# Kernel tuning notes

Hardware: AMD Instinct MI355X
Metric: run time of the kernel (lower is better)

The kernel has to match this reference:

```python
import jax, jax.numpy as jnp
import numpy as np

EPS = 1e-5

def instance_norm(x):
    # x: [B, n, C]; InstanceNorm1d normalizes over the n (length) axis per channel, no affine
    mean = jnp.mean(x, axis=1, keepdims=True)
    var = jnp.var(x, axis=1, keepdims=True)  # biased variance, matches torch
    return (x - mean) / jnp.sqrt(var + EPS)

def gat_layer(h, w, a_src, a_dst, b):
    # h: [B, n, d_in]; w: [H, d_in, d_out]; a_src/a_dst: [H, d_out, 1]; b: [d_out]
    h_ = jnp.einsum('bnd,hdk->bhnk', h, w)               # [B, H, n, d_out]
    s_src = jnp.einsum('bhnk,hk->bhn', h_, a_src[..., 0])  # [B, H, n]
    s_dst = jnp.einsum('bhnk,hk->bhn', h_, a_dst[..., 0])  # [B, H, n]
    attn = s_src[:, :, :, None] + s_dst[:, :, None, :]    # [B, H, n, n]
    attn = jax.nn.leaky_relu(attn, negative_slope=0.2)
    attn = jax.nn.softmax(attn, axis=-1)
    return jnp.einsum('bhnm,bhmk->bhnk', attn, h_) + b    # [B, H, n, d_out]

def setup_inputs() -> dict:
    key = jax.random.key(0)
    ks = jax.random.split(key, 7)
    B, N = 4, 4096
    x = jax.random.normal(ks[0], (B, N, 64), dtype=jnp.float32)
    g = 1.414
    def xavier(k, shape):
        fan_in, fan_out = shape[-2], shape[-1]
        lim = g * np.sqrt(6.0 / (fan_in + fan_out))
        return jax.random.uniform(k, shape, jnp.float32, -lim, lim)
    return {
        'x': x,
        'w0': xavier(ks[1], (4, 64, 32)),
        'a_src0': xavier(ks[2], (4, 32, 1)),
        'a_dst0': xavier(ks[3], (4, 32, 1)),
        'b0': jnp.zeros((32,), jnp.float32),
        'w1': xavier(ks[4], (1, 128, 64)),
        'a_src1': xavier(ks[5], (1, 64, 1)),
        'a_dst1': xavier(ks[6], (1, 64, 1)),
        'b1': jnp.zeros((64,), jnp.float32),
    }

def reference(x, w0, a_src0, a_dst0, b0, w1, a_src1, a_dst1, b1):
    B, N = x.shape[:2]
    # layer 0: norm -> GAT(4 heads) -> concat heads -> ELU
    h = instance_norm(x)
    h = gat_layer(h, w0, a_src0, a_dst0, b0)              # [B, 4, N, 32]
    h = jnp.transpose(h, (0, 2, 1, 3)).reshape(B, N, -1)  # [B, N, 128]
    h = jax.nn.elu(h)
    # layer 1: norm -> GAT(1 head) -> squeeze head
    h = instance_norm(h)
    h = gat_layer(h, w1, a_src1, a_dst1, b1)              # [B, 1, N, 64]
    return h[:, 0]                                        # [B, N, 64]
```

## Files before the change

kernel.cpp:

```cpp
#include <hip/hip_runtime.h>
#include <math.h>

#define N_ 4096

static constexpr size_t OFF_STATS0 = 0;
static constexpr size_t OFF_STATS1 = 512;
static constexpr size_t OFF_HP0    = 2048;
static constexpr size_t OFF_ELU    = 2048;
static constexpr size_t OFF_SS0    = 2099200;
static constexpr size_t OFF_SD0    = 2164736;
static constexpr size_t OFF_RUNS0  = 2230272;
static constexpr size_t OFF_SV0    = 2361344;
static constexpr size_t OFF_PM0    = 2426880;
static constexpr size_t OFF_EP0    = 2492416;
static constexpr size_t OFF_EN0    = 2557952;
static constexpr size_t OFF_CPP0   = 2623488;
static constexpr size_t OFF_CPN0   = 2689040;
static constexpr size_t OFF_RAWP0  = 2754592;
static constexpr size_t OFF_RAWN0  = 2885664;
static constexpr size_t OFF_BP0    = 3016736;
static constexpr size_t OFF_BN0    = 3148320;
static constexpr size_t OFF_TPP0   = 3279904;
static constexpr size_t OFF_TPN0   = 5377568;
static constexpr size_t OFF_HP1    = 3279904;
static constexpr size_t OFF_SS1    = 4328480;
static constexpr size_t OFF_SD1    = 4344864;
static constexpr size_t OFF_RUNS1  = 4361248;
static constexpr size_t OFF_SV1    = 4394016;
static constexpr size_t OFF_PM1    = 4410400;
static constexpr size_t OFF_EP1    = 4426784;
static constexpr size_t OFF_EN1    = 4443168;
static constexpr size_t OFF_CPP1   = 4459552;
static constexpr size_t OFF_CPN1   = 4475940;
static constexpr size_t OFF_RAWP1  = 4492328;
static constexpr size_t OFF_RAWN1  = 4557864;
static constexpr size_t OFF_BP1    = 4623400;
static constexpr size_t OFF_BN1    = 4689192;
static constexpr size_t OFF_TPP1   = 4754984;
static constexpr size_t OFF_TPN1   = 5803816;

__device__ __forceinline__ unsigned f2s(float f){
  unsigned u=__float_as_uint(f);
  return u^((u&0x80000000u)?0xFFFFFFFFu:0x80000000u);
}
__device__ __forceinline__ float s2f(unsigned s){
  unsigned u=(s&0x80000000u)?(s^0x80000000u):~s;
  return __uint_as_float(u);
}

template<int C>
__global__ void kstats(const float* __restrict__ x, float* __restrict__ stats){
  int blk=blockIdx.x; int b=blk>>5, seg=blk&31;
  int tid=threadIdx.x;
  const int RPT=256/C;
  const int IT=128/RPT;
  int c=tid%C, rl=tid/C;
  const float* xb=x+(size_t)b*N_*C;
  float s1=0.f,s2=0.f;
  int r0=seg*128+rl;
  for(int i=0;i<IT;i++){
    float v=xb[(size_t)(r0+i*RPT)*C+c];
    s1+=v;s2+=v*v;
  }
  __shared__ float sh1[256],sh2[256];
  sh1[tid]=s1;sh2[tid]=s2;__syncthreads();
  if(tid<C){
    float a1=0.f,a2=0.f;
    for(int g=0;g<RPT;g++){a1+=sh1[g*C+tid];a2+=sh2[g*C+tid];}
    atomicAdd(&stats[(size_t)(b*C+tid)*2+0],a1);
    atomicAdd(&stats[(size_t)(b*C+tid)*2+1],a2);
  }
}

__global__ void __launch_bounds__(256) kproj0(
                       const float* __restrict__ x, const float* __restrict__ stats,
                       const float* __restrict__ w0, const float* __restrict__ asrc,
                       const float* __restrict__ adst, float* __restrict__ hp,
                       float* __restrict__ ss, float* __restrict__ sd){
  __shared__ float4 w4[2048];
  __shared__ float4 av4[64];
  __shared__ float mean[64],rstd[64];
  int tid=threadIdx.x;
  const float4* wg=(const float4*)w0;
  for(int i=tid;i<2048;i+=256) w4[i]=wg[i];
  if(tid<32) av4[tid]=((const float4*)asrc)[tid];
  else if(tid<64) av4[tid]=((const float4*)adst)[tid-32];
  int gid=blockIdx.x*256+tid;
  int b=gid>>14, h=(gid>>12)&3, n=gid&4095;
  if(tid<64){
    float s1=stats[(size_t)(b*64+tid)*2+0],s2=stats[(size_t)(b*64+tid)*2+1];
    float mu=s1*(1.0f/N_);
    float var=s2*(1.0f/N_)-mu*mu;
    mean[tid]=mu; rstd[tid]=rsqrtf(var+1e-5f);
  }
  __syncthreads();
  const float4* hr4=(const float4*)(x+((size_t)(b*N_+n))*64);
  float4 acc[8];
  #pragma unroll
  for(int q=0;q<8;q++) acc[q]=make_float4(0.f,0.f,0.f,0.f);
  #pragma unroll
  for(int ch=0;ch<4;ch++){
    float4 t[4];
    #pragma unroll
    for(int j=0;j<4;j++) t[j]=hr4[ch*4+j];
    #pragma unroll
    for(int j=0;j<4;j++){
      int d0=ch*16+j*4;
      float hv[4];
      hv[0]=(t[j].x-mean[d0+0])*rstd[d0+0];
      hv[1]=(t[j].y-mean[d0+1])*rstd[d0+1];
      hv[2]=(t[j].z-mean[d0+2])*rstd[d0+2];
      hv[3]=(t[j].w-mean[d0+3])*rstd[d0+3];
      #pragma unroll
      for(int dd=0;dd<4;dd++){
        float hvv=hv[dd];
        #pragma unroll
        for(int q=0;q<8;q++){
          float4 wv=w4[(h*64+d0+dd)*8+q];
          acc[q].x+=hvv*wv.x;acc[q].y+=hvv*wv.y;acc[q].z+=hvv*wv.z;acc[q].w+=hvv*wv.w;
        }
      }
    }
  }
  float ssv=0.f,sdv=0.f;
  #pragma unroll
  for(int q=0;q<8;q++){
    float4 a1=av4[h*8+q],a2=av4[32+h*8+q];
    ssv+=acc[q].x*a1.x+acc[q].y*a1.y+acc[q].z*a1.z+acc[q].w*a1.w;
    sdv+=acc[q].x*a2.x+acc[q].y*a2.y+acc[q].z*a2.z+acc[q].w*a2.w;
  }
  int p=b*4+h;
  float4* o4=(float4*)(hp+((size_t)p*N_+n)*32);
  #pragma unroll
  for(int q=0;q<8;q++) o4[q]=acc[q];
  ss[(size_t)p*N_+n]=ssv; sd[(size_t)p*N_+n]=sdv;
}

__global__ void __launch_bounds__(256) kproj1(
                       const float* __restrict__ x, const float* __restrict__ stats,
                       const float* __restrict__ w1, const float* __restrict__ asrc,
                       const float* __restrict__ adst, float* __restrict__ hp,
                       float* __restrict__ ss, float* __restrict__ sd){
  __shared__ float4 w4[2048];
  __shared__ float wa[128],wd[128],mean[128],rstd[128];
  int tid=threadIdx.x;
  const float4* wg=(const float4*)w1;
  for(int i=tid;i<2048;i+=256) w4[i]=wg[i];
  int gid=blockIdx.x*256+tid;
  int b=gid>>14, q4=(gid>>12)&3, n=gid&4095;
  if(tid<128){
    float s1a=0.f,s2a=0.f;
    for(int k=0;k<64;k++){float wv=w1[tid*64+k];s1a+=wv*asrc[k];s2a+=wv*adst[k];}
    wa[tid]=s1a;wd[tid]=s2a;
    float s1=stats[(size_t)(b*128+tid)*2+0],s2=stats[(size_t)(b*128+tid)*2+1];
    float mu=s1*(1.0f/N_);
    float var=s2*(1.0f/N_)-mu*mu;
    mean[tid]=mu; rstd[tid]=rsqrtf(var+1e-5f);
  }
  __syncthreads();
  const float4* hr4=(const float4*)(x+((size_t)(b*N_+n))*128);
  float4 acc[4];
  #pragma unroll
  for(int q=0;q<4;q++) acc[q]=make_float4(0.f,0.f,0.f,0.f);
  float s1=0.f,s2=0.f;
  #pragma unroll
  for(int ch=0;ch<8;ch++){
    float4 t[4];
    #pragma unroll
    for(int j=0;j<4;j++) t[j]=hr4[ch*4+j];
    #pragma unroll
    for(int j=0;j<4;j++){
      int d0=ch*16+j*4;
      float hv[4];
      hv[0]=(t[j].x-mean[d0+0])*rstd[d0+0];
      hv[1]=(t[j].y-mean[d0+1])*rstd[d0+1];
      hv[2]=(t[j].z-mean[d0+2])*rstd[d0+2];
      hv[3]=(t[j].w-mean[d0+3])*rstd[d0+3];
      #pragma unroll
      for(int dd=0;dd<4;dd++){
        float hvv=hv[dd]; int d=d0+dd;
        s1+=hvv*wa[d]; s2+=hvv*wd[d];
        #pragma unroll
        for(int q=0;q<4;q++){
          float4 wv=w4[d*16+q4*4+q];
          acc[q].x+=hvv*wv.x;acc[q].y+=hvv*wv.y;acc[q].z+=hvv*wv.z;acc[q].w+=hvv*wv.w;
        }
      }
    }
  }
  float4* o4=(float4*)(hp+((size_t)(b*N_+n))*64+q4*16);
  #pragma unroll
  for(int q=0;q<4;q++) o4[q]=acc[q];
  if(q4==0){
    ss[(size_t)b*N_+n]=s1;sd[(size_t)b*N_+n]=s2;
  }
}

__global__ void __launch_bounds__(256) ksort_runs(const float* __restrict__ sdst,
                                                  unsigned long long* __restrict__ runs){
  __shared__ unsigned long long sm[1024];
  int p=blockIdx.x>>2, run=blockIdx.x&3;
  int tid=threadIdx.x;
  const float* s=sdst+(size_t)p*N_+run*1024;
  for(int l=tid;l<1024;l+=256){
    unsigned key=f2s(s[l]);
    sm[l]=((unsigned long long)key<<32)|(unsigned)(run*1024+l);
  }
  for(unsigned k=2;k<=1024u;k<<=1)
    for(unsigned j=k>>1;j>0;j>>=1){
      __syncthreads();
      for(unsigned t=tid;t<512u;t+=256u){
        unsigned i=((t&~(j-1))<<1)|(t&(j-1));
        unsigned q=i|j;
        bool up=((i&k)==0);
        unsigned long long a=sm[i],b=sm[q];
        if((a>b)==up){sm[i]=b;sm[q]=a;}
      }
    }
  __syncthreads();
  unsigned long long* rg=runs+(size_t)p*N_+run*1024;
  for(int l=tid;l<1024;l+=256) rg[l]=sm[l];
}

__global__ void __launch_bounds__(1024) kmerge(const unsigned long long* __restrict__ runs,
    float* __restrict__ sv, unsigned* __restrict__ perm,
    float* __restrict__ eP, float* __restrict__ eN){
  __shared__ unsigned long long sm[4096];
  int p=blockIdx.x>>2, cg=blockIdx.x&3;
  int tid=threadIdx.x;
  const unsigned long long* rg=runs+(size_t)p*N_;
  for(int l=tid;l<4096;l+=1024) sm[l]=rg[l];
  __syncthreads();
  unsigned long long e=sm[cg*1024+tid];
  int rank=tid;
  #pragma unroll
  for(int o=0;o<4;o++){
    if(o==cg) continue;
    const unsigned long long* base=sm+o*1024;
    int lo=0,hi=1024;
    while(lo<hi){int mid=(lo+hi)>>1; if(base[mid]<e) lo=mid+1; else hi=mid;}
    rank+=lo;
  }
  unsigned long long mk=sm[1023];
  if(sm[2047]>mk) mk=sm[2047];
  if(sm[3071]>mk) mk=sm[3071];
  if(sm[4095]>mk) mk=sm[4095];
  float m=s2f((unsigned)(mk>>32));
  float v=s2f((unsigned)(e>>32));
  size_t o=(size_t)p*N_+rank;
  sv[o]=v;
  perm[o]=(unsigned)(e&0xffffffffu);
  eP[o]=expf(v-m);
  eN[o]=expf(0.2f*(v-m));
}

__global__ void __launch_bounds__(1024) kcounts(const float* __restrict__ eP,
    const float* __restrict__ eN, float* __restrict__ CPP, float* __restrict__ CPN){
  __shared__ float sp[1024],sn[1024];
  int p=blockIdx.x, t=threadIdx.x;
  float4 e4=((const float4*)(eP+(size_t)p*N_))[t];
  float4 n4=((const float4*)(eN+(size_t)p*N_))[t];
  float lp=e4.x+e4.y+e4.z+e4.w;
  float ln=n4.x+n4.y+n4.z+n4.w;
  sp[t]=lp; sn[t]=ln; __syncthreads();
  for(int off=1;off<1024;off<<=1){
    float vp=(t>=off)?sp[t-off]:0.f;
    float vn=(t>=off)?sn[t-off]:0.f;
    __syncthreads();
    sp[t]+=vp; sn[t]+=vn;
    __syncthreads();
  }
  float bp=sp[t]-lp, bn=sn[t]-ln;
  size_t o=(size_t)p*4097+t*4;
  float a=bp;          CPP[o+0]=a;
  a+=e4.x;             CPP[o+1]=a;
  a+=e4.y;             CPP[o+2]=a;
  a+=e4.z;             CPP[o+3]=a;
  a=bn;                CPN[o+0]=a;
  a+=n4.x;             CPN[o+1]=a;
  a+=n4.y;             CPN[o+2]=a;
  a+=n4.z;             CPN[o+3]=a;
  if(t==1023){CPP[(size_t)p*4097+4096]=sp[1023]; CPN[(size_t)p*4097+4096]=sn[1023];}
}

__global__ void __launch_bounds__(256) ktables0(const unsigned* __restrict__ perm,
    const float* __restrict__ eP, const float* __restrict__ eN,
    const float* __restrict__ hp, float* __restrict__ TPP, float* __restrict__ TPN,
    float* __restrict__ rawP, float* __restrict__ rawN){
  int gw=(blockIdx.x*256+threadIdx.x)>>6;
  int lane=threadIdx.x&63, half=lane>>5, ch=lane&31;
  int cglob=gw*2+half;
  int p=cglob>>8, c=cglob&255;
  float aP=0.f,aN=0.f;
  for(int q=0;q<16;q++){
    int r=c*16+q;
    size_t ro=(size_t)p*N_+r;
    float ep=eP[ro],en=eN[ro];
    unsigned pr=perm[ro];
    float hv=hp[((size_t)p*N_+pr)*32+ch];
    size_t to=((size_t)p*4097+r)*32+ch;
    TPP[to]=aP; TPN[to]=aN;
    aP+=ep*hv; aN+=en*hv;
  }
  size_t bo=((size_t)p*256+c)*32+ch;
  rawP[bo]=aP; rawN[bo]=aN;
}

__global__ void __launch_bounds__(256) ktables1(const unsigned* __restrict__ perm,
    const float* __restrict__ eP, const float* __restrict__ eN,
    const float* __restrict__ hp, float* __restrict__ TPP, float* __restrict__ TPN,
    float* __restrict__ rawP, float* __restrict__ rawN){
  int wid=(blockIdx.x*256+threadIdx.x)>>6;
  int lane=threadIdx.x&63;
  int p=wid>>8, c=wid&255;
  float aP=0.f,aN=0.f;
  for(int q=0;q<16;q++){
    int r=c*16+q;
    size_t ro=(size_t)p*N_+r;
    float ep=eP[ro],en=eN[ro];
    unsigned pr=perm[ro];
    float hv=hp[((size_t)p*N_+pr)*64+lane];
    size_t to=((size_t)p*4097+r)*64+lane;
    TPP[to]=aP; TPN[to]=aN;
    aP+=ep*hv; aN+=en*hv;
  }
  size_t bo=((size_t)p*256+c)*64+lane;
  rawP[bo]=aP; rawN[bo]=aN;
}

template<int D>
__global__ void __launch_bounds__(256) kscan(const float* __restrict__ rawP,
    const float* __restrict__ rawN, float* __restrict__ bP, float* __restrict__ bN,
    float* __restrict__ TPP, float* __restrict__ TPN){
  extern __shared__ float sm[];
  int p=blockIdx.x, tid=threadIdx.x;
  for(int pass=0;pass<2;pass++){
    const float* src=pass?rawN:rawP;
    float* dst=pass?bN:bP;
    float* tp=pass?TPN:TPP;
    __syncthreads();
    for(int i=tid;i<256*D;i+=256){
      sm[i]=src[(size_t)p*256*D+i];
    }
    __syncthreads();
    if(tid<D){
      float r=0.f;
      for(int c=0;c<256;c++){
        dst[((size_t)p*257+c)*D+tid]=r;
        r+=sm[c*D+tid];
      }
      dst[((size_t)p*257+256)*D+tid]=0.f;
      tp[((size_t)p*4097+4096)*D+tid]=r;
    }
  }
}

__global__ void __launch_bounds__(256) keval0(const float* __restrict__ ss,
                       const float* __restrict__ sv,
                       const float* __restrict__ bP, const float* __restrict__ bN,
                       const float* __restrict__ TPP, const float* __restrict__ TPN,
                       const float* __restrict__ CPP, const float* __restrict__ CPN,
                       const float* __restrict__ bias, float* __restrict__ out){
  int gw=(blockIdx.x*256+threadIdx.x)>>6;
  int lane=threadIdx.x&63, half=lane>>5, ch=lane&31;
  int row=gw*2+half;
  int p=row>>12, i=row&4095;
  int b=p>>2, h=p&3;
  const float* svp=sv+(size_t)p*N_;
  float ssrc=ss[(size_t)p*N_+i];
  float m=svp[4095];
  float xx=ssrc+m;
  float M=xx>0.f?xx:0.2f*xx;
  float fpos=expf(xx-M),fneg=expf(0.2f*xx-M);
  float th=-ssrc;
  float s1v=svp[ch*128+127];
  unsigned long long bal=__ballot(s1v<=th);
  int c1=half?(int)__popcll(bal>>32):(int)__popcll(bal&0xFFFFFFFFull);
  int lo;
  if(c1>=32){ lo=4096; }
  else{
    float s2v=svp[c1*128+ch*4+3];
    unsigned long long bal2=__ballot(s2v<=th);
    int c2=half?(int)__popcll(bal2>>32):(int)__popcll(bal2&0xFFFFFFFFull);
    int base=c1*128+c2*4;
    float4 qv=*((const float4*)(svp+base));
    int c3=(qv.x<=th)+(qv.y<=th)+(qv.z<=th)+(qv.w<=th);
    lo=base+c3;
  }
  int c=lo>>4;
  float relP=TPP[((size_t)p*4097+lo)*32+ch];
  float relN=TPN[((size_t)p*4097+lo)*32+ch];
  float baP=bP[((size_t)p*257+c)*32+ch];
  float baN=bN[((size_t)p*257+c)*32+ch];
  float tot=TPP[((size_t)p*4097+4096)*32+ch];
  float CPl=CPP[(size_t)p*4097+lo];
  float CNl=CPN[(size_t)p*4097+lo];
  float CT =CPP[(size_t)p*4097+4096];
  float denom=fpos*(CT-CPl)+fneg*CNl;
  float v=fpos*(tot-(baP+relP))+fneg*(baN+relN);
  float r=v/denom+bias[ch];
  r=r>0.f?r:expm1f(r);
  out[((size_t)(b*N_+i))*128+h*32+ch]=r;
}

__global__ void __launch_bounds__(256) keval1(const float* __restrict__ ss,
                       const float* __restrict__ sv,
                       const float* __restrict__ bP, const float* __restrict__ bN,
                       const float* __restrict__ TPP, const float* __restrict__ TPN,
                       const float* __restrict__ CPP, const float* __restrict__ CPN,
                       const float* __restrict__ bias, float* __restrict__ out){
  int wid=(blockIdx.x*256+threadIdx.x)>>6;
  int lane=threadIdx.x&63;
  int p=wid>>12, i=wid&4095;
  const float* svp=sv+(size_t)p*N_;
  float ssrc=ss[(size_t)p*N_+i];
  float m=svp[4095];
  float xx=ssrc+m;
  float M=xx>0.f?xx:0.2f*xx;
  float fpos=expf(xx-M),fneg=expf(0.2f*xx-M);
  float th=-ssrc;
  float s1v=svp[lane*64+63];
  int c1=(int)__popcll(__ballot(s1v<=th));
  int lo;
  if(c1>=64){ lo=4096; }
  else{
    float s2v=svp[c1*64+lane];
    lo=c1*64+(int)__popcll(__ballot(s2v<=th));
  }
  int c=lo>>4;
  float relP=TPP[((size_t)p*4097+lo)*64+lane];
  float relN=TPN[((size_t)p*4097+lo)*64+lane];
  float baP=bP[((size_t)p*257+c)*64+lane];
  float baN=bN[((size_t)p*257+c)*64+lane];
  float tot=TPP[((size_t)p*4097+4096)*64+lane];
  float CPl=CPP[(size_t)p*4097+lo];
  float CNl=CPN[(size_t)p*4097+lo];
  float CT =CPP[(size_t)p*4097+4096];
  float denom=fpos*(CT-CPl)+fneg*CNl;
  float v=fpos*(tot-(baP+relP))+fneg*(baN+relN);
  out[((size_t)p*N_+i)*64+lane]=v/denom+bias[lane];
}

extern "C" void kernel_launch(void* const* d_in, const int* in_sizes, int n_in,
                              void* d_out, int out_size, void* d_ws, size_t ws_size,
                              hipStream_t stream) {
  const float* x  =(const float*)d_in[0];
  const float* w0 =(const float*)d_in[1];
  const float* as0=(const float*)d_in[2];
  const float* ad0=(const float*)d_in[3];
  const float* b0 =(const float*)d_in[4];
  const float* w1 =(const float*)d_in[5];
  const float* as1=(const float*)d_in[6];
  const float* ad1=(const float*)d_in[7];
  const float* b1 =(const float*)d_in[8];
  float* ws=(float*)d_ws;
  float* out=(float*)d_out;

  float* st0 = ws+OFF_STATS0;
  float* st1 = ws+OFF_STATS1;
  float* hp0 = ws+OFF_HP0;
  float* elu = ws+OFF_ELU;
  float* ss0 = ws+OFF_SS0;  float* sd0 = ws+OFF_SD0;
  unsigned long long* runs0=(unsigned long long*)(ws+OFF_RUNS0);
  float* sv0 = ws+OFF_SV0;
  unsigned* pm0=(unsigned*)(ws+OFF_PM0);
  float* eP0 = ws+OFF_EP0;  float* eN0 = ws+OFF_EN0;
  float* cP0 = ws+OFF_CPP0; float* cN0 = ws+OFF_CPN0;
  float* rP0 = ws+OFF_RAWP0; float* rN0 = ws+OFF_RAWN0;
  float* bP0 = ws+OFF_BP0;  float* bN0 = ws+OFF_BN0;
  float* tP0 = ws+OFF_TPP0; float* tN0 = ws+OFF_TPN0;
  float* hp1 = ws+OFF_HP1;
  float* ss1 = ws+OFF_SS1;  float* sd1 = ws+OFF_SD1;
  unsigned long long* runs1=(unsigned long long*)(ws+OFF_RUNS1);
  float* sv1 = ws+OFF_SV1;
  unsigned* pm1=(unsigned*)(ws+OFF_PM1);
  float* eP1 = ws+OFF_EP1;  float* eN1 = ws+OFF_EN1;
  float* cP1 = ws+OFF_CPP1; float* cN1 = ws+OFF_CPN1;
  float* rP1 = ws+OFF_RAWP1; float* rN1 = ws+OFF_RAWN1;
  float* bP1 = ws+OFF_BP1;  float* bN1 = ws+OFF_BN1;
  float* tP1 = ws+OFF_TPP1; float* tN1 = ws+OFF_TPN1;

  hipMemsetAsync(d_ws, 0, 1536*sizeof(float), stream);

  kstats<64><<<128,256,0,stream>>>(x,st0);
  kproj0<<<256,256,0,stream>>>(x,st0,w0,as0,ad0,hp0,ss0,sd0);
  ksort_runs<<<64,256,0,stream>>>(sd0,runs0);
  kmerge<<<64,1024,0,stream>>>(runs0,sv0,pm0,eP0,eN0);
  kcounts<<<16,1024,0,stream>>>(eP0,eN0,cP0,cN0);
  ktables0<<<512,256,0,stream>>>(pm0,eP0,eN0,hp0,tP0,tN0,rP0,rN0);
  kscan<32><<<16,256,256*32*4,stream>>>(rP0,rN0,bP0,bN0,tP0,tN0);
  keval0<<<8192,256,0,stream>>>(ss0,sv0,bP0,bN0,tP0,tN0,cP0,cN0,b0,elu);
  kstats<128><<<128,256,0,stream>>>(elu,st1);
  kproj1<<<256,256,0,stream>>>(elu,st1,w1,as1,ad1,hp1,ss1,sd1);
  ksort_runs<<<16,256,0,stream>>>(sd1,runs1);
  kmerge<<<16,1024,0,stream>>>(runs1,sv1,pm1,eP1,eN1);
  kcounts<<<4,1024,0,stream>>>(eP1,eN1,cP1,cN1);
  ktables1<<<256,256,0,stream>>>(pm1,eP1,eN1,hp1,tP1,tN1,rP1,rN1);
  kscan<64><<<4,256,256*64*4,stream>>>(rP1,rN1,bP1,bN1,tP1,tN1);
  keval1<<<4096,256,0,stream>>>(ss1,sv1,bP1,bN1,tP1,tN1,cP1,cN1,b1,out);
}
```

Before: 233.2 us.

## Fuse count prefix sums into kscan, stats1 into keval0, two rows per projection thread

Removes the separate kcounts kernel and computes the eP/eN prefix sums inside kscan. It also drops the layer-1 kstats pass by accumulating per-channel sums and squares in keval0 through block reduction and atomics. The projection kernels now handle two nodes per thread on half the blocks, so each LDS weight read is reused twice. This saves kernel launches and a full re-read of the ELU output, at the cost of more atomics in keval0 and fewer, heavier blocks in the projections.

```diff
diff --git a/kernel.cpp b/kernel.cpp
--- a/kernel.cpp
+++ b/kernel.cpp
@@ -86,7 +86,7 @@
   if(tid<32) av4[tid]=((const float4*)asrc)[tid];
   else if(tid<64) av4[tid]=((const float4*)adst)[tid-32];
   int gid=blockIdx.x*256+tid;
-  int b=gid>>14, h=(gid>>12)&3, n=gid&4095;
+  int b=gid>>13, h=(gid>>11)&3, n0=gid&2047;
   if(tid<64){
     float s1=stats[(size_t)(b*64+tid)*2+0],s2=stats[(size_t)(b*64+tid)*2+1];
     float mu=s1*(1.0f/N_);
@@ -94,46 +94,52 @@
     mean[tid]=mu; rstd[tid]=rsqrtf(var+1e-5f);
   }
   __syncthreads();
-  const float4* hr4=(const float4*)(x+((size_t)(b*N_+n))*64);
-  float4 acc[8];
-  #pragma unroll
-  for(int q=0;q<8;q++) acc[q]=make_float4(0.f,0.f,0.f,0.f);
+  const float4* hA4=(const float4*)(x+((size_t)(b*N_+n0))*64);
+  const float4* hB4=(const float4*)(x+((size_t)(b*N_+n0+2048))*64);
+  float4 accA[8],accB[8];
+  #pragma unroll
+  for(int q=0;q<8;q++){accA[q]=make_float4(0.f,0.f,0.f,0.f);accB[q]=make_float4(0.f,0.f,0.f,0.f);}
   #pragma unroll
   for(int ch=0;ch<4;ch++){
-    float4 t[4];
+    float4 tA[4],tB[4];
     #pragma unroll
-    for(int j=0;j<4;j++) t[j]=hr4[ch*4+j];
+    for(int j=0;j<4;j++){tA[j]=hA4[ch*4+j];tB[j]=hB4[ch*4+j];}
     #pragma unroll
     for(int j=0;j<4;j++){
       int d0=ch*16+j*4;
-      float hv[4];
-      hv[0]=(t[j].x-mean[d0+0])*rstd[d0+0];
-      hv[1]=(t[j].y-mean[d0+1])*rstd[d0+1];
-      hv[2]=(t[j].z-mean[d0+2])*rstd[d0+2];
-      hv[3]=(t[j].w-mean[d0+3])*rstd[d0+3];
+      float hvA[4],hvB[4];
+      hvA[0]=(tA[j].x-mean[d0+0])*rstd[d0+0]; hvB[0]=(tB[j].x-mean[d0+0])*rstd[d0+0];
+      hvA[1]=(tA[j].y-mean[d0+1])*rstd[d0+1]; hvB[1]=(tB[j].y-mean[d0+1])*rstd[d0+1];
+      hvA[2]=(tA[j].z-mean[d0+2])*rstd[d0+2]; hvB[2]=(tB[j].z-mean[d0+2])*rstd[d0+2];
+      hvA[3]=(tA[j].w-mean[d0+3])*rstd[d0+3]; hvB[3]=(tB[j].w-mean[d0+3])*rstd[d0+3];
       #pragma unroll
       for(int dd=0;dd<4;dd++){
-        float hvv=hv[dd];
+        float a=hvA[dd],bb=hvB[dd];
         #pragma unroll
         for(int q=0;q<8;q++){
           float4 wv=w4[(h*64+d0+dd)*8+q];
-          acc[q].x+=hvv*wv.x;acc[q].y+=hvv*wv.y;acc[q].z+=hvv*wv.z;acc[q].w+=hvv*wv.w;
+          accA[q].x+=a*wv.x;accA[q].y+=a*wv.y;accA[q].z+=a*wv.z;accA[q].w+=a*wv.w;
+          accB[q].x+=bb*wv.x;accB[q].y+=bb*wv.y;accB[q].z+=bb*wv.z;accB[q].w+=bb*wv.w;
         }
       }
     }
   }
-  float ssv=0.f,sdv=0.f;
+  float ssA=0.f,sdA=0.f,ssB=0.f,sdB=0.f;
   #pragma unroll
   for(int q=0;q<8;q++){
     float4 a1=av4[h*8+q],a2=av4[32+h*8+q];
-    ssv+=acc[q].x*a1.x+acc[q].y*a1.y+acc[q].z*a1.z+acc[q].w*a1.w;
-    sdv+=acc[q].x*a2.x+acc[q].y*a2.y+acc[q].z*a2.z+acc[q].w*a2.w;
+    ssA+=accA[q].x*a1.x+accA[q].y*a1.y+accA[q].z*a1.z+accA[q].w*a1.w;
+    sdA+=accA[q].x*a2.x+accA[q].y*a2.y+accA[q].z*a2.z+accA[q].w*a2.w;
+    ssB+=accB[q].x*a1.x+accB[q].y*a1.y+accB[q].z*a1.z+accB[q].w*a1.w;
+    sdB+=accB[q].x*a2.x+accB[q].y*a2.y+accB[q].z*a2.z+accB[q].w*a2.w;
   }
   int p=b*4+h;
-  float4* o4=(float4*)(hp+((size_t)p*N_+n)*32);
-  #pragma unroll
-  for(int q=0;q<8;q++) o4[q]=acc[q];
-  ss[(size_t)p*N_+n]=ssv; sd[(size_t)p*N_+n]=sdv;
+  float4* oA=(float4*)(hp+((size_t)p*N_+n0)*32);
+  float4* oB=(float4*)(hp+((size_t)p*N_+n0+2048)*32);
+  #pragma unroll
+  for(int q=0;q<8;q++){oA[q]=accA[q];oB[q]=accB[q];}
+  ss[(size_t)p*N_+n0]=ssA; sd[(size_t)p*N_+n0]=sdA;
+  ss[(size_t)p*N_+n0+2048]=ssB; sd[(size_t)p*N_+n0+2048]=sdB;
 }
 
 __global__ void __launch_bounds__(256) kproj1(
@@ -147,7 +153,7 @@
   const float4* wg=(const float4*)w1;
   for(int i=tid;i<2048;i+=256) w4[i]=wg[i];
   int gid=blockIdx.x*256+tid;
-  int b=gid>>14, q4=(gid>>12)&3, n=gid&4095;
+  int b=gid>>13, q4=(gid>>11)&3, n0=gid&2047;
   if(tid<128){
     float s1a=0.f,s2a=0.f;
     for(int k=0;k<64;k++){float wv=w1[tid*64+k];s1a+=wv*asrc[k];s2a+=wv*adst[k];}
@@ -158,41 +164,46 @@
     mean[tid]=mu; rstd[tid]=rsqrtf(var+1e-5f);
   }
   __syncthreads();
-  const float4* hr4=(const float4*)(x+((size_t)(b*N_+n))*128);
-  float4 acc[4];
-  #pragma unroll
-  for(int q=0;q<4;q++) acc[q]=make_float4(0.f,0.f,0.f,0.f);
-  float s1=0.f,s2=0.f;
+  const float4* hA4=(const float4*)(x+((size_t)(b*N_+n0))*128);
+  const float4* hB4=(const float4*)(x+((size_t)(b*N_+n0+2048))*128);
+  float4 accA[4],accB[4];
+  #pragma unroll
+  for(int q=0;q<4;q++){accA[q]=make_float4(0.f,0.f,0.f,0.f);accB[q]=make_float4(0.f,0.f,0.f,0.f);}
+  float s1A=0.f,s2A=0.f,s1B=0.f,s2B=0.f;
   #pragma unroll
   for(int ch=0;ch<8;ch++){
-    float4 t[4];
+    float4 tA[4],tB[4];
     #pragma unroll
-    for(int j=0;j<4;j++) t[j]=hr4[ch*4+j];
+    for(int j=0;j<4;j++){tA[j]=hA4[ch*4+j];tB[j]=hB4[ch*4+j];}
     #pragma unroll
     for(int j=0;j<4;j++){
       int d0=ch*16+j*4;
-      float hv[4];
-      hv[0]=(t[j].x-mean[d0+0])*rstd[d0+0];
-      hv[1]=(t[j].y-mean[d0+1])*rstd[d0+1];
-      hv[2]=(t[j].z-mean[d0+2])*rstd[d0+2];
-      hv[3]=(t[j].w-mean[d0+3])*rstd[d0+3];
+      float hvA[4],hvB[4];
+      hvA[0]=(tA[j].x-mean[d0+0])*rstd[d0+0]; hvB[0]=(tB[j].x-mean[d0+0])*rstd[d0+0];
+      hvA[1]=(tA[j].y-mean[d0+1])*rstd[d0+1]; hvB[1]=(tB[j].y-mean[d0+1])*rstd[d0+1];
+      hvA[2]=(tA[j].z-mean[d0+2])*rstd[d0+2]; hvB[2]=(tB[j].z-mean[d0+2])*rstd[d0+2];
+      hvA[3]=(tA[j].w-mean[d0+3])*rstd[d0+3]; hvB[3]=(tB[j].w-mean[d0+3])*rstd[d0+3];
       #pragma unroll
       for(int dd=0;dd<4;dd++){
-        float hvv=hv[dd]; int d=d0+dd;
-        s1+=hvv*wa[d]; s2+=hvv*wd[d];
+        float a=hvA[dd],bb=hvB[dd]; int d=d0+dd;
+        s1A+=a*wa[d]; s2A+=a*wd[d];
+        s1B+=bb*wa[d]; s2B+=bb*wd[d];
         #pragma unroll
         for(int q=0;q<4;q++){
           float4 wv=w4[d*16+q4*4+q];
-          acc[q].x+=hvv*wv.x;acc[q].y+=hvv*wv.y;acc[q].z+=hvv*wv.z;acc[q].w+=hvv*wv.w;
+          accA[q].x+=a*wv.x;accA[q].y+=a*wv.y;accA[q].z+=a*wv.z;accA[q].w+=a*wv.w;
+          accB[q].x+=bb*wv.x;accB[q].y+=bb*wv.y;accB[q].z+=bb*wv.z;accB[q].w+=bb*wv.w;
         }
       }
     }
   }
-  float4* o4=(float4*)(hp+((size_t)(b*N_+n))*64+q4*16);
-  #pragma unroll
-  for(int q=0;q<4;q++) o4[q]=acc[q];
+  float4* oA=(float4*)(hp+((size_t)(b*N_+n0))*64+q4*16);
+  float4* oB=(float4*)(hp+((size_t)(b*N_+n0+2048))*64+q4*16);
+  #pragma unroll
+  for(int q=0;q<4;q++){oA[q]=accA[q];oB[q]=accB[q];}
   if(q4==0){
-    ss[(size_t)b*N_+n]=s1;sd[(size_t)b*N_+n]=s2;
+    ss[(size_t)b*N_+n0]=s1A; sd[(size_t)b*N_+n0]=s2A;
+    ss[(size_t)b*N_+n0+2048]=s1B; sd[(size_t)b*N_+n0+2048]=s2B;
   }
 }
 
@@ -252,35 +263,6 @@
   perm[o]=(unsigned)(e&0xffffffffu);
   eP[o]=expf(v-m);
   eN[o]=expf(0.2f*(v-m));
-}
-
-__global__ void __launch_bounds__(1024) kcounts(const float* __restrict__ eP,
-    const float* __restrict__ eN, float* __restrict__ CPP, float* __restrict__ CPN){
-  __shared__ float sp[1024],sn[1024];
-  int p=blockIdx.x, t=threadIdx.x;
-  float4 e4=((const float4*)(eP+(size_t)p*N_))[t];
-  float4 n4=((const float4*)(eN+(size_t)p*N_))[t];
-  float lp=e4.x+e4.y+e4.z+e4.w;
-  float ln=n4.x+n4.y+n4.z+n4.w;
-  sp[t]=lp; sn[t]=ln; __syncthreads();
-  for(int off=1;off<1024;off<<=1){
-    float vp=(t>=off)?sp[t-off]:0.f;
-    float vn=(t>=off)?sn[t-off]:0.f;
-    __syncthreads();
-    sp[t]+=vp; sn[t]+=vn;
-    __syncthreads();
-  }
-  float bp=sp[t]-lp, bn=sn[t]-ln;
-  size_t o=(size_t)p*4097+t*4;
-  float a=bp;          CPP[o+0]=a;
-  a+=e4.x;             CPP[o+1]=a;
-  a+=e4.y;             CPP[o+2]=a;
-  a+=e4.z;             CPP[o+3]=a;
-  a=bn;                CPN[o+0]=a;
-  a+=n4.x;             CPN[o+1]=a;
-  a+=n4.y;             CPN[o+2]=a;
-  a+=n4.z;             CPN[o+3]=a;
-  if(t==1023){CPP[(size_t)p*4097+4096]=sp[1023]; CPN[(size_t)p*4097+4096]=sn[1023];}
 }
 
 __global__ void __launch_bounds__(256) ktables0(const unsigned* __restrict__ perm,
@@ -331,7 +313,9 @@
 template<int D>
 __global__ void __launch_bounds__(256) kscan(const float* __restrict__ rawP,
     const float* __restrict__ rawN, float* __restrict__ bP, float* __restrict__ bN,
-    float* __restrict__ TPP, float* __restrict__ TPN){
+    float* __restrict__ TPP, float* __restrict__ TPN,
+    const float* __restrict__ eP, const float* __restrict__ eN,
+    float* __restrict__ CPP, float* __restrict__ CPN){
   extern __shared__ float sm[];
   int p=blockIdx.x, tid=threadIdx.x;
   for(int pass=0;pass<2;pass++){
@@ -339,9 +323,7 @@
     float* dst=pass?bN:bP;
     float* tp=pass?TPN:TPP;
     __syncthreads();
-    for(int i=tid;i<256*D;i+=256){
-      sm[i]=src[(size_t)p*256*D+i];
-    }
+    for(int i=tid;i<256*D;i+=256) sm[i]=src[(size_t)p*256*D+i];
     __syncthreads();
     if(tid<D){
       float r=0.f;
@@ -353,6 +335,29 @@
       tp[((size_t)p*4097+4096)*D+tid]=r;
     }
   }
+  for(int pass=0;pass<2;pass++){
+    const float* src=pass?eN:eP;
+    float* dst=pass?CPN:CPP;
+    __syncthreads();
+    for(int i=tid;i<1024;i+=256) ((float4*)sm)[i]=((const float4*)(src+(size_t)p*N_))[i];
+    __syncthreads();
+    float part=0.f;
+    for(int j=0;j<16;j++) part+=sm[tid*16+j];
+    sm[4096+tid]=part;
+    __syncthreads();
+    for(int off=1;off<256;off<<=1){
+      float v=(tid>=off)?sm[4096+tid-off]:0.f;
+      __syncthreads();
+      sm[4096+tid]+=v;
+      __syncthreads();
+    }
+    float a=sm[4096+tid]-part;
+    for(int j=0;j<16;j++){
+      dst[(size_t)p*4097+tid*16+j]=a;
+      a+=sm[tid*16+j];
+    }
+    if(tid==255) dst[(size_t)p*4097+4096]=sm[4096+255];
+  }
 }
 
 __global__ void __launch_bounds__(256) keval0(const float* __restrict__ ss,
@@ -360,7 +365,8 @@
                        const float* __restrict__ bP, const float* __restrict__ bN,
                        const float* __restrict__ TPP, const float* __restrict__ TPN,
                        const float* __restrict__ CPP, const float* __restrict__ CPN,
-                       const float* __restrict__ bias, float* __restrict__ out){
+                       const float* __restrict__ bias, float* __restrict__ out,
+                       float* __restrict__ stats1){
   int gw=(blockIdx.x*256+threadIdx.x)>>6;
   int lane=threadIdx.x&63, half=lane>>5, ch=lane&31;
   int row=gw*2+half;
@@ -401,6 +407,18 @@
   float r=v/denom+bias[ch];
   r=r>0.f?r:expm1f(r);
   out[((size_t)(b*N_+i))*128+h*32+ch]=r;
+  __shared__ float shS[256],shQ[256];
+  shS[threadIdx.x]=r; shQ[threadIdx.x]=r*r;
+  __syncthreads();
+  if(threadIdx.x<32){
+    float s=0.f,q=0.f;
+    #pragma unroll
+    for(int k=0;k<8;k++){s+=shS[threadIdx.x+32*k];q+=shQ[threadIdx.x+32*k];}
+    int row0=blockIdx.x*8;
+    int p0=row0>>12; int b0=p0>>2,h0=p0&3;
+    atomicAdd(&stats1[(size_t)(b0*128+h0*32+threadIdx.x)*2+0],s);
+    atomicAdd(&stats1[(size_t)(b0*128+h0*32+threadIdx.x)*2+1],q);
+  }
 }
 
 __global__ void __launch_bounds__(256) keval1(const float* __restrict__ ss,
@@ -483,19 +501,16 @@
   hipMemsetAsync(d_ws, 0, 1536*sizeof(float), stream);
 
   kstats<64><<<128,256,0,stream>>>(x,st0);
-  kproj0<<<256,256,0,stream>>>(x,st0,w0,as0,ad0,hp0,ss0,sd0);
+  kproj0<<<128,256,0,stream>>>(x,st0,w0,as0,ad0,hp0,ss0,sd0);
   ksort_runs<<<64,256,0,stream>>>(sd0,runs0);
   kmerge<<<64,1024,0,stream>>>(runs0,sv0,pm0,eP0,eN0);
-  kcounts<<<16,1024,0,stream>>>(eP0,eN0,cP0,cN0);
   ktables0<<<512,256,0,stream>>>(pm0,eP0,eN0,hp0,tP0,tN0,rP0,rN0);
-  kscan<32><<<16,256,256*32*4,stream>>>(rP0,rN0,bP0,bN0,tP0,tN0);
-  keval0<<<8192,256,0,stream>>>(ss0,sv0,bP0,bN0,tP0,tN0,cP0,cN0,b0,elu);
-  kstats<128><<<128,256,0,stream>>>(elu,st1);
-  kproj1<<<256,256,0,stream>>>(elu,st1,w1,as1,ad1,hp1,ss1,sd1);
+  kscan<32><<<16,256,256*32*4,stream>>>(rP0,rN0,bP0,bN0,tP0,tN0,eP0,eN0,cP0,cN0);
+  keval0<<<8192,256,0,stream>>>(ss0,sv0,bP0,bN0,tP0,tN0,cP0,cN0,b0,elu,st1);
+  kproj1<<<128,256,0,stream>>>(elu,st1,w1,as1,ad1,hp1,ss1,sd1);
   ksort_runs<<<16,256,0,stream>>>(sd1,runs1);
   kmerge<<<16,1024,0,stream>>>(runs1,sv1,pm1,eP1,eN1);
-  kcounts<<<4,1024,0,stream>>>(eP1,eN1,cP1,cN1);
   ktables1<<<256,256,0,stream>>>(pm1,eP1,eN1,hp1,tP1,tN1,rP1,rN1);
-  kscan<64><<<4,256,256*64*4,stream>>>(rP1,rN1,bP1,bN1,tP1,tN1);
+  kscan<64><<<4,256,256*64*4,stream>>>(rP1,rN1,bP1,bN1,tP1,tN1,eP1,eN1,cP1,cN1);
   keval1<<<4096,256,0,stream>>>(ss1,sv1,bP1,bN1,tP1,tN1,cP1,cN1,b1,out);
 }
```

Measured after the change: 333.6 us. +43.1%, slower.

## Fuse prefix counts into scan kernel and layer-1 stats into eval0

Applied to the files above, without the earlier changes.

The separate kcounts kernel is removed, and the prefix sums of eP/eN are now computed at the end of kscan using shared memory. The instance-norm statistics for layer 1 are now gathered inside keval0: each block reduces sum and sum-of-squares per channel and adds them into stats1 with atomics, which replaces the kstats<128> pass. This cuts kernel launches and drops one full re-read of the ELU output. In exchange it adds heavy atomic contention on a small set of addresses and makes the float summation order nondeterministic.

```diff
diff --git a/kernel.cpp b/kernel.cpp
--- a/kernel.cpp
+++ b/kernel.cpp
@@ -254,35 +254,6 @@
   eN[o]=expf(0.2f*(v-m));
 }
 
-__global__ void __launch_bounds__(1024) kcounts(const float* __restrict__ eP,
-    const float* __restrict__ eN, float* __restrict__ CPP, float* __restrict__ CPN){
-  __shared__ float sp[1024],sn[1024];
-  int p=blockIdx.x, t=threadIdx.x;
-  float4 e4=((const float4*)(eP+(size_t)p*N_))[t];
-  float4 n4=((const float4*)(eN+(size_t)p*N_))[t];
-  float lp=e4.x+e4.y+e4.z+e4.w;
-  float ln=n4.x+n4.y+n4.z+n4.w;
-  sp[t]=lp; sn[t]=ln; __syncthreads();
-  for(int off=1;off<1024;off<<=1){
-    float vp=(t>=off)?sp[t-off]:0.f;
-    float vn=(t>=off)?sn[t-off]:0.f;
-    __syncthreads();
-    sp[t]+=vp; sn[t]+=vn;
-    __syncthreads();
-  }
-  float bp=sp[t]-lp, bn=sn[t]-ln;
-  size_t o=(size_t)p*4097+t*4;
-  float a=bp;          CPP[o+0]=a;
-  a+=e4.x;             CPP[o+1]=a;
-  a+=e4.y;             CPP[o+2]=a;
-  a+=e4.z;             CPP[o+3]=a;
-  a=bn;                CPN[o+0]=a;
-  a+=n4.x;             CPN[o+1]=a;
-  a+=n4.y;             CPN[o+2]=a;
-  a+=n4.z;             CPN[o+3]=a;
-  if(t==1023){CPP[(size_t)p*4097+4096]=sp[1023]; CPN[(size_t)p*4097+4096]=sn[1023];}
-}
-
 __global__ void __launch_bounds__(256) ktables0(const unsigned* __restrict__ perm,
     const float* __restrict__ eP, const float* __restrict__ eN,
     const float* __restrict__ hp, float* __restrict__ TPP, float* __restrict__ TPN,
@@ -331,7 +302,9 @@
 template<int D>
 __global__ void __launch_bounds__(256) kscan(const float* __restrict__ rawP,
     const float* __restrict__ rawN, float* __restrict__ bP, float* __restrict__ bN,
-    float* __restrict__ TPP, float* __restrict__ TPN){
+    float* __restrict__ TPP, float* __restrict__ TPN,
+    const float* __restrict__ eP, const float* __restrict__ eN,
+    float* __restrict__ CPP, float* __restrict__ CPN){
   extern __shared__ float sm[];
   int p=blockIdx.x, tid=threadIdx.x;
   for(int pass=0;pass<2;pass++){
@@ -339,9 +312,7 @@
     float* dst=pass?bN:bP;
     float* tp=pass?TPN:TPP;
     __syncthreads();
-    for(int i=tid;i<256*D;i+=256){
-      sm[i]=src[(size_t)p*256*D+i];
-    }
+    for(int i=tid;i<256*D;i+=256) sm[i]=src[(size_t)p*256*D+i];
     __syncthreads();
     if(tid<D){
       float r=0.f;
@@ -353,6 +324,29 @@
       tp[((size_t)p*4097+4096)*D+tid]=r;
     }
   }
+  for(int pass=0;pass<2;pass++){
+    const float* src=pass?eN:eP;
+    float* dst=pass?CPN:CPP;
+    __syncthreads();
+    for(int i=tid;i<1024;i+=256) ((float4*)sm)[i]=((const float4*)(src+(size_t)p*N_))[i];
+    __syncthreads();
+    float part=0.f;
+    for(int j=0;j<16;j++) part+=sm[tid*16+j];
+    sm[4096+tid]=part;
+    __syncthreads();
+    for(int off=1;off<256;off<<=1){
+      float v=(tid>=off)?sm[4096+tid-off]:0.f;
+      __syncthreads();
+      sm[4096+tid]+=v;
+      __syncthreads();
+    }
+    float a=sm[4096+tid]-part;
+    for(int j=0;j<16;j++){
+      dst[(size_t)p*4097+tid*16+j]=a;
+      a+=sm[tid*16+j];
+    }
+    if(tid==255) dst[(size_t)p*4097+4096]=sm[4096+255];
+  }
 }
 
 __global__ void __launch_bounds__(256) keval0(const float* __restrict__ ss,
@@ -360,7 +354,8 @@
                        const float* __restrict__ bP, const float* __restrict__ bN,
                        const float* __restrict__ TPP, const float* __restrict__ TPN,
                        const float* __restrict__ CPP, const float* __restrict__ CPN,
-                       const float* __restrict__ bias, float* __restrict__ out){
+                       const float* __restrict__ bias, float* __restrict__ out,
+                       float* __restrict__ stats1){
   int gw=(blockIdx.x*256+threadIdx.x)>>6;
   int lane=threadIdx.x&63, half=lane>>5, ch=lane&31;
   int row=gw*2+half;
@@ -401,6 +396,18 @@
   float r=v/denom+bias[ch];
   r=r>0.f?r:expm1f(r);
   out[((size_t)(b*N_+i))*128+h*32+ch]=r;
+  __shared__ float shS[256],shQ[256];
+  shS[threadIdx.x]=r; shQ[threadIdx.x]=r*r;
+  __syncthreads();
+  if(threadIdx.x<32){
+    float s=0.f,q=0.f;
+    #pragma unroll
+    for(int k=0;k<8;k++){s+=shS[threadIdx.x+32*k];q+=shQ[threadIdx.x+32*k];}
+    int row0=blockIdx.x*8;
+    int p0=row0>>12; int b0=p0>>2,h0=p0&3;
+    atomicAdd(&stats1[(size_t)(b0*128+h0*32+threadIdx.x)*2+0],s);
+    atomicAdd(&stats1[(size_t)(b0*128+h0*32+threadIdx.x)*2+1],q);
+  }
 }
 
 __global__ void __launch_bounds__(256) keval1(const float* __restrict__ ss,
@@ -486,16 +493,13 @@
   kproj0<<<256,256,0,stream>>>(x,st0,w0,as0,ad0,hp0,ss0,sd0);
   ksort_runs<<<64,256,0,stream>>>(sd0,runs0);
   kmerge<<<64,1024,0,stream>>>(runs0,sv0,pm0,eP0,eN0);
-  kcounts<<<16,1024,0,stream>>>(eP0,eN0,cP0,cN0);
   ktables0<<<512,256,0,stream>>>(pm0,eP0,eN0,hp0,tP0,tN0,rP0,rN0);
-  kscan<32><<<16,256,256*32*4,stream>>>(rP0,rN0,bP0,bN0,tP0,tN0);
-  keval0<<<8192,256,0,stream>>>(ss0,sv0,bP0,bN0,tP0,tN0,cP0,cN0,b0,elu);
-  kstats<128><<<128,256,0,stream>>>(elu,st1);
+  kscan<32><<<16,256,256*32*4,stream>>>(rP0,rN0,bP0,bN0,tP0,tN0,eP0,eN0,cP0,cN0);
+  keval0<<<8192,256,0,stream>>>(ss0,sv0,bP0,bN0,tP0,tN0,cP0,cN0,b0,elu,st1);
   kproj1<<<256,256,0,stream>>>(elu,st1,w1,as1,ad1,hp1,ss1,sd1);
   ksort_runs<<<16,256,0,stream>>>(sd1,runs1);
   kmerge<<<16,1024,0,stream>>>(runs1,sv1,pm1,eP1,eN1);
-  kcounts<<<4,1024,0,stream>>>(eP1,eN1,cP1,cN1);
   ktables1<<<256,256,0,stream>>>(pm1,eP1,eN1,hp1,tP1,tN1,rP1,rN1);
-  kscan<64><<<4,256,256*64*4,stream>>>(rP1,rN1,bP1,bN1,tP1,tN1);
+  kscan<64><<<4,256,256*64*4,stream>>>(rP1,rN1,bP1,bN1,tP1,tN1,eP1,eN1,cP1,cN1);
   keval1<<<4096,256,0,stream>>>(ss1,sv1,bP1,bN1,tP1,tN1,cP1,cN1,b1,out);
 }
```

Measured after the change: 282.1 us. 21.0% more time.
